# Performance work log

Measured on AMD Instinct MI355X. Metric: run time of the kernel, lower is better.

Reference implementation:

```python
import jax, jax.numpy as jnp
import numpy as np

B, T, C = 16, 512, 32
W = 128            # max_window
SERIES_LEN = 100000
WIN_MIN, WIN_MAX = 2.0, 64.0
SHARP = 1.0        # fixed sharpness of the soft window edge
BN_EPS = 1e-5


def setup_inputs() -> dict:
    key = jax.random.key(0)
    ks = jax.random.split(key, 6)
    x = jax.random.normal(ks[0], (B, T, C), jnp.float32)
    full_series = jax.random.normal(ks[1], (SERIES_LEN, C), jnp.float32)
    # starts >= W so the lookback window never needs padding; end = start + T
    starts = jax.random.randint(ks[2], (B,), W, SERIES_LEN - T)
    indices = jnp.stack([starts, starts + T], axis=1).astype(jnp.int32)  # (B, 2)
    # raw (logit-space) per-channel window sizes, as in the torch init
    raw_win_mean = jax.random.normal(ks[3], (C,), jnp.float32)
    raw_win_std = jax.random.normal(ks[4], (C,), jnp.float32)
    return dict(
        x=x, full_series=full_series, indices=indices,
        raw_win_mean=raw_win_mean, raw_win_std=raw_win_std,
        gamma_mean=jnp.ones((C,), jnp.float32), beta_mean=jnp.zeros((C,), jnp.float32),
        gamma_std=jnp.ones((C,), jnp.float32), beta_std=jnp.zeros((C,), jnp.float32),
    )


def _soft_window_weights(raw_win):
    # sigmoid-mapped window size in [WIN_MIN, WIN_MAX], per channel
    win = WIN_MIN + jax.nn.sigmoid(raw_win) * (WIN_MAX - WIN_MIN)          # (C,)
    age = jnp.arange(W, dtype=jnp.float32)[::-1]                            # slot W-1 is most recent (age 0)
    w = jax.nn.sigmoid(SHARP * (win[None, :] - age[:, None]))               # (W, C)
    return w


def _rolling_windows(full_series, starts):
    # batch_windows[b] = full_series[starts[b]-W : starts[b]+T]   -> (B, W+T, C)
    offs = jnp.arange(W + T)
    bw = full_series[(starts - W)[:, None] + offs[None, :]]                 # (B, W+T, C)
    # window for output step t covers slots [t, t+W) (the W points before the current step)
    tidx = jnp.arange(T)[:, None] + jnp.arange(W)[None, :]                  # (T, W)
    return bw[:, tidx, :]                                                   # (B, T, W, C)


def _batchnorm(f, gamma, beta):
    # BatchNorm1d over (B, C, T): normalize per channel over batch and time, biased var
    mean = f.mean(axis=(0, 1))
    var = ((f - mean) ** 2).mean(axis=(0, 1))
    return (f - mean) * jax.lax.rsqrt(var + BN_EPS) * gamma + beta


def reference(x, full_series, indices, raw_win_mean, raw_win_std,
              gamma_mean, beta_mean, gamma_std, beta_std):
    starts = indices[:, 0]
    xw = _rolling_windows(full_series, starts)                              # (B, T, W, C)

    # feature 1: soft-window weighted mean
    w1 = _soft_window_weights(raw_win_mean)                                 # (W, C)
    s1 = jnp.sum(w1, axis=0)                                                # (C,)
    f_mean = jnp.einsum('btwc,wc->btc', xw, w1) / s1                        # (B, T, C)

    # feature 2: soft-window weighted std
    w2 = _soft_window_weights(raw_win_std)
    s2 = jnp.sum(w2, axis=0)
    m2 = jnp.einsum('btwc,wc->btc', xw, w2) / s2
    var2 = jnp.einsum('btwc,wc->btc', (xw - m2[:, :, None, :]) ** 2, w2) / s2
    f_std = jnp.sqrt(var2 + 1e-8)

    out_mean = _batchnorm(f_mean, gamma_mean, beta_mean)
    out_std = _batchnorm(f_std, gamma_std, beta_std)
    return jnp.concatenate([x, out_mean, out_std], axis=-1)                 # (B, T, 3*C)
```

## Files before the change

### kernel.cpp

```cpp
#include <hip/hip_runtime.h>
#include <math.h>

#define NB 16
#define NT 512
#define NC 32
#define NW 128
#define TILE_T 32
#define NTILES (NT / TILE_T)
#define NBLK (NB * NTILES)
#define NROWS (TILE_T + NW)
#define PADROWS 169
#define NTR 25
#define WIN_MIN_F 2.0f
#define WIN_RANGE_F 62.0f

#define WS_FMEAN 0
#define WS_FSTD  (NB*NT*NC)
#define WS_PART  (2*NB*NT*NC)

typedef float v2f __attribute__((ext_vector_type(2)));

__device__ __forceinline__ float fast_sigmoid_neg(float a) {
    return __builtin_amdgcn_rcpf(1.0f + __expf(a));
}

__global__ __launch_bounds__(256) void feat_main(
    const float* __restrict__ x,
    const float* __restrict__ series,
    const int*   __restrict__ indices,
    const float* __restrict__ rwm,
    const float* __restrict__ rws,
    float* __restrict__ f_mean,
    float* __restrict__ f_std,
    float* __restrict__ partials,
    float* __restrict__ out)
{
    __shared__ __align__(16) float s_x[PADROWS * NC];
    __shared__ __align__(16) v2f   s_P[NROWS * NC];
    __shared__ __align__(16) v2f   s_wt[NTR * NC];
    __shared__ float s_win[2 * NC];
    __shared__ int   s_wsi[2 * NC];
    __shared__ float s_red[1024];

    const int tid = threadIdx.x;
    const int blk = blockIdx.x;
    const int b   = blk >> 4;
    const int tt  = blk & 15;
    const int t0  = tt * TILE_T;
    const int start = indices[2 * b];

    {
        const int row = b * NT + t0 + (tid >> 3);
        const int q = tid & 7;
        ((float4*)out)[row * 24 + q] = ((const float4*)x)[row * 8 + q];
    }

    if (tid < 2 * NC) {
        const int c = tid & 31;
        const float raw = (tid < NC) ? rwm[c] : rws[c];
        const float win = WIN_MIN_F + WIN_RANGE_F * fast_sigmoid_neg(-raw);
        s_win[tid] = win;
        s_wsi[tid] = (int)(115.0f - win);
    }

    const float4* src4 = (const float4*)(series + (size_t)(start - NW + t0) * NC);
    float4* dst4 = (float4*)s_x;
#pragma unroll
    for (int k = 0; k < 5; ++k) {
        const int j = tid + k * 256;
        dst4[j] = src4[j];
    }
    if (tid < 72) {
        dst4[1280 + tid] = make_float4(0.f, 0.f, 0.f, 0.f);
    }
    __syncthreads();

    const int c_s  = tid & 31;
    const int seg  = tid >> 5;
    float l1[20], l2[20];
    {
        float r1 = 0.f, r2 = 0.f;
        const int base = (seg * 20) * NC + c_s;
#pragma unroll
        for (int i = 0; i < 20; ++i) {
            l1[i] = r1; l2[i] = r2;
            const float xv = s_x[base + i * NC];
            r1 += xv;
            r2 = fmaf(xv, xv, r2);
        }
        s_red[0 * 256 + seg * NC + c_s] = r1;
        s_red[1 * 256 + seg * NC + c_s] = r2;
    }

    for (int i = tid; i < 2 * NTR * NC; i += 256) {
        const int c = i & 31;
        const int r = i >> 5;
        const int tbl = (r >= NTR) ? 1 : 0;
        const int j = r - NTR * tbl;
        const int ws = s_wsi[tbl * NC + c];
        const int w = ws + j;
        float val = 0.f;
        if (w < NW) {
            const float age = (float)(NW - 1 - w);
            val = fast_sigmoid_neg(age - s_win[tbl * NC + c]);
        }
        ((float*)s_wt)[(j * NC + c) * 2 + tbl] = val;
    }
    __syncthreads();

    if (tid < 64) {
        const int tbl = tid >> 5, c = tid & 31;
        float o = 0.f;
#pragma unroll
        for (int s = 0; s < 8; ++s) {
            const int idx = tbl * 256 + s * NC + c;
            const float t = s_red[idx];
            s_red[idx] = o;
            o += t;
        }
    }
    __syncthreads();

    {
        const float o1 = s_red[0 * 256 + seg * NC + c_s];
        const float o2 = s_red[1 * 256 + seg * NC + c_s];
#pragma unroll
        for (int i = 0; i < 20; ++i) {
            v2f p; p.x = o1 + l1[i]; p.y = o2 + l2[i];
            s_P[(seg * 20 + i) * NC + c_s] = p;
        }
    }
    __syncthreads();

    const int c  = tid & 31;
    const int rg = tid >> 5;
    const int r0 = rg * 4;
    const int wsm = s_wsi[c];
    const int wss = s_wsi[NC + c];

    float a1[4] = {0.f,0.f,0.f,0.f};
    float a2[4] = {0.f,0.f,0.f,0.f};
    float a3[4] = {0.f,0.f,0.f,0.f};
    float sw1 = 0.f, sw2 = 0.f;

    const int bm_ = (r0 + wsm) * NC + c;
    const int bs_ = (r0 + wss) * NC + c;
    float xm[4], xv[4], qv[4];
#pragma unroll
    for (int k = 0; k < 4; ++k) {
        xm[k] = s_x[bm_ + k * NC];
        const float v = s_x[bs_ + k * NC];
        xv[k] = v; qv[k] = v * v;
    }

#pragma unroll 5
    for (int j = 0; j < NTR; ++j) {
        const v2f wv = s_wt[j * NC + c];
        sw1 += wv.x; sw2 += wv.y;
#pragma unroll
        for (int k = 0; k < 4; ++k) {
            a1[k] = fmaf(xm[k], wv.x, a1[k]);
            a2[k] = fmaf(xv[k], wv.y, a2[k]);
            a3[k] = fmaf(qv[k], wv.y, a3[k]);
        }
        xm[0] = xm[1]; xm[1] = xm[2]; xm[2] = xm[3];
        xm[3] = s_x[bm_ + (4 + j) * NC];
        xv[0] = xv[1]; xv[1] = xv[2]; xv[2] = xv[3];
        qv[0] = qv[1]; qv[1] = qv[2]; qv[2] = qv[3];
        const float nv = s_x[bs_ + (4 + j) * NC];
        xv[3] = nv; qv[3] = nv * nv;
    }

    const int wsm25 = (wsm + NTR < NW) ? wsm + NTR : NW;
    const int wss25 = (wss + NTR < NW) ? wss + NTR : NW;
    const float s1 = sw1 + (float)(NW - wsm25);
    const float s2 = sw2 + (float)(NW - wss25);
    const float inv1 = __builtin_amdgcn_rcpf(s1);
    const float inv2 = __builtin_amdgcn_rcpf(s2);

    float p0 = 0.f, p1 = 0.f, p2 = 0.f, p3 = 0.f;
#pragma unroll
    for (int k = 0; k < 4; ++k) {
        const int t = r0 + k;
        const v2f pe = s_P[(t + NW) * NC + c];
        const v2f pm = s_P[(t + wsm25) * NC + c];
        const v2f ps = s_P[(t + wss25) * NC + c];
        const float A1 = a1[k] + (pe.x - pm.x);
        const float A2 = a2[k] + (pe.x - ps.x);
        const float A3 = a3[k] + (pe.y - ps.y);
        const float fm = A1 * inv1;
        const float m2 = A2 * inv2;
        const float var = fmaxf(A3 * inv2 - m2 * m2, 0.f);
        const float fs = sqrtf(var + 1e-8f);
        const size_t o = ((size_t)(b * NT + t0 + t)) * NC + c;
        f_mean[o] = fm;
        f_std[o]  = fs;
        p0 += fm; p1 = fmaf(fm, fm, p1); p2 += fs; p3 = fmaf(fs, fs, p3);
    }

    s_red[0 * 256 + rg * NC + c] = p0;
    s_red[1 * 256 + rg * NC + c] = p1;
    s_red[2 * 256 + rg * NC + c] = p2;
    s_red[3 * 256 + rg * NC + c] = p3;
    __syncthreads();

    if (tid < 128) {
        const int stat = tid >> 5, cc = tid & 31;
        float s = 0.f;
#pragma unroll
        for (int g = 0; g < 8; ++g) s += s_red[stat * 256 + g * NC + cc];
        partials[blk * (4 * NC) + stat * NC + cc] = s;
    }
}

__global__ __launch_bounds__(256) void bn_write(
    const float* __restrict__ f_mean,
    const float* __restrict__ f_std,
    const float* __restrict__ partials,
    const float* __restrict__ gm, const float* __restrict__ bm,
    const float* __restrict__ gs, const float* __restrict__ bs,
    float* __restrict__ out)
{
    __shared__ __align__(16) float s_part[8 * 128];
    __shared__ __align__(16) float s_sums[128];
    __shared__ __align__(16) float s_coef[4 * NC];

    const int tid = threadIdx.x;

    {
        const int cell  = tid & 31;
        const int slice = tid >> 5;
        const float4* p4 = (const float4*)partials;
        float4 acc = {0.f, 0.f, 0.f, 0.f};
#pragma unroll 8
        for (int i = 0; i < 32; ++i) {
            const float4 v = p4[(slice * 32 + i) * 32 + cell];
            acc.x += v.x; acc.y += v.y; acc.z += v.z; acc.w += v.w;
        }
        *(float4*)&s_part[(slice * 32 + cell) * 4] = acc;
    }
    __syncthreads();
    if (tid < 32) {
        float4 s = {0.f, 0.f, 0.f, 0.f};
#pragma unroll
        for (int sl = 0; sl < 8; ++sl) {
            const float4 v = ((const float4*)s_part)[sl * 32 + tid];
            s.x += v.x; s.y += v.y; s.z += v.z; s.w += v.w;
        }
        ((float4*)s_sums)[tid] = s;
    }
    __syncthreads();
    if (tid < NC) {
        const float invN = 1.0f / (float)(NB * NT);
        const float mu_m  = s_sums[tid] * invN;
        float var_m = s_sums[32 + tid] * invN - mu_m * mu_m;
        var_m = fmaxf(var_m, 0.0f);
        const float A1 = gm[tid] / sqrtf(var_m + 1e-5f);
        const float B1 = bm[tid] - mu_m * A1;
        const float mu_s  = s_sums[64 + tid] * invN;
        float var_s = s_sums[96 + tid] * invN - mu_s * mu_s;
        var_s = fmaxf(var_s, 0.0f);
        const float A2 = gs[tid] / sqrtf(var_s + 1e-5f);
        const float B2 = bs[tid] - mu_s * A2;
        s_coef[tid]          = A1;
        s_coef[NC + tid]     = B1;
        s_coef[2 * NC + tid] = A2;
        s_coef[3 * NC + tid] = B2;
    }
    __syncthreads();

    const float4* fm4 = (const float4*)f_mean;
    const float4* fs4 = (const float4*)f_std;
    const float4* cf4 = (const float4*)s_coef;
    float4* out4 = (float4*)out;
    const int row0 = blockIdx.x * 32;

#pragma unroll
    for (int k = 0; k < 2; ++k) {
        const int j = tid + k * 256;
        const int r = j >> 4;
        const int q = j & 15;
        const int row = row0 + r;
        float4 v;
        int oq;
        if (q < 8) {
            const float4 f = fm4[row * 8 + q];
            const float4 A = cf4[q], Bv = cf4[8 + q];
            v.x = fmaf(f.x, A.x, Bv.x); v.y = fmaf(f.y, A.y, Bv.y);
            v.z = fmaf(f.z, A.z, Bv.z); v.w = fmaf(f.w, A.w, Bv.w);
            oq = 8 + q;
        } else {
            const int m = q - 8;
            const float4 f = fs4[row * 8 + m];
            const float4 A = cf4[16 + m], Bv = cf4[24 + m];
            v.x = fmaf(f.x, A.x, Bv.x); v.y = fmaf(f.y, A.y, Bv.y);
            v.z = fmaf(f.z, A.z, Bv.z); v.w = fmaf(f.w, A.w, Bv.w);
            oq = 16 + m;
        }
        out4[row * 24 + oq] = v;
    }
}

extern "C" void kernel_launch(void* const* d_in, const int* in_sizes, int n_in,
                              void* d_out, int out_size, void* d_ws, size_t ws_size,
                              hipStream_t stream) {
    const float* x      = (const float*)d_in[0];
    const float* series = (const float*)d_in[1];
    const int*   idx    = (const int*)d_in[2];
    const float* rwm    = (const float*)d_in[3];
    const float* rws    = (const float*)d_in[4];
    const float* gm     = (const float*)d_in[5];
    const float* bm     = (const float*)d_in[6];
    const float* gs     = (const float*)d_in[7];
    const float* bs     = (const float*)d_in[8];
    float* out = (float*)d_out;
    float* ws  = (float*)d_ws;

    float* f_mean   = ws + WS_FMEAN;
    float* f_std    = ws + WS_FSTD;
    float* partials = ws + WS_PART;

    feat_main<<<NBLK, 256, 0, stream>>>(x, series, idx, rwm, rws, f_mean, f_std, partials, out);
    bn_write<<<NBLK, 256, 0, stream>>>(f_mean, f_std, partials, gm, bm, gs, bs, out);
}
```

Measured before the change: 15.08 us.

## Fuse feature and batchnorm kernels via grid-wide atomic barrier

New measurement: 30.61 us. 2.03x slower.

```diff
diff --git a/kernel.cpp b/kernel.cpp
--- a/kernel.cpp
+++ b/kernel.cpp
@@ -14,25 +14,22 @@
 #define WIN_MIN_F 2.0f
 #define WIN_RANGE_F 62.0f
 
-#define WS_FMEAN 0
-#define WS_FSTD  (NB*NT*NC)
-#define WS_PART  (2*NB*NT*NC)
-
 typedef float v2f __attribute__((ext_vector_type(2)));
 
 __device__ __forceinline__ float fast_sigmoid_neg(float a) {
     return __builtin_amdgcn_rcpf(1.0f + __expf(a));
 }
 
-__global__ __launch_bounds__(256) void feat_main(
+__global__ __launch_bounds__(256) void feat_fused(
     const float* __restrict__ x,
     const float* __restrict__ series,
     const int*   __restrict__ indices,
     const float* __restrict__ rwm,
     const float* __restrict__ rws,
-    float* __restrict__ f_mean,
-    float* __restrict__ f_std,
+    const float* __restrict__ gm, const float* __restrict__ bm,
+    const float* __restrict__ gs, const float* __restrict__ bs,
     float* __restrict__ partials,
+    unsigned int* __restrict__ ctr,
     float* __restrict__ out)
 {
     __shared__ __align__(16) float s_x[PADROWS * NC];
@@ -40,7 +37,9 @@
     __shared__ __align__(16) v2f   s_wt[NTR * NC];
     __shared__ float s_win[2 * NC];
     __shared__ int   s_wsi[2 * NC];
-    __shared__ float s_red[1024];
+    __shared__ __align__(16) float s_red[1024];
+    __shared__ __align__(16) float s_sums[128];
+    __shared__ __align__(16) float s_coef[128];
 
     const int tid = threadIdx.x;
     const int blk = blockIdx.x;
@@ -178,6 +177,7 @@
     const float inv1 = __builtin_amdgcn_rcpf(s1);
     const float inv2 = __builtin_amdgcn_rcpf(s2);
 
+    float fm[4], fs[4];
     float p0 = 0.f, p1 = 0.f, p2 = 0.f, p3 = 0.f;
 #pragma unroll
     for (int k = 0; k < 4; ++k) {
@@ -188,14 +188,11 @@
         const float A1 = a1[k] + (pe.x - pm.x);
         const float A2 = a2[k] + (pe.x - ps.x);
         const float A3 = a3[k] + (pe.y - ps.y);
-        const float fm = A1 * inv1;
+        fm[k] = A1 * inv1;
         const float m2 = A2 * inv2;
         const float var = fmaxf(A3 * inv2 - m2 * m2, 0.f);
-        const float fs = sqrtf(var + 1e-8f);
-        const size_t o = ((size_t)(b * NT + t0 + t)) * NC + c;
-        f_mean[o] = fm;
-        f_std[o]  = fs;
-        p0 += fm; p1 = fmaf(fm, fm, p1); p2 += fs; p3 = fmaf(fs, fs, p3);
+        fs[k] = sqrtf(var + 1e-8f);
+        p0 += fm[k]; p1 = fmaf(fm[k], fm[k], p1); p2 += fs[k]; p3 = fmaf(fs[k], fs[k], p3);
     }
 
     s_red[0 * 256 + rg * NC + c] = p0;
@@ -211,21 +208,17 @@
         for (int g = 0; g < 8; ++g) s += s_red[stat * 256 + g * NC + cc];
         partials[blk * (4 * NC) + stat * NC + cc] = s;
     }
-}
-
-__global__ __launch_bounds__(256) void bn_write(
-    const float* __restrict__ f_mean,
-    const float* __restrict__ f_std,
-    const float* __restrict__ partials,
-    const float* __restrict__ gm, const float* __restrict__ bm,
-    const float* __restrict__ gs, const float* __restrict__ bs,
-    float* __restrict__ out)
-{
-    __shared__ __align__(16) float s_part[8 * 128];
-    __shared__ __align__(16) float s_sums[128];
-    __shared__ __align__(16) float s_coef[4 * NC];
-
-    const int tid = threadIdx.x;
+    __syncthreads();
+
+    if (tid == 0) {
+        __hip_atomic_fetch_add(ctr, 1u, __ATOMIC_ACQ_REL, __HIP_MEMORY_SCOPE_AGENT);
+        unsigned int guard = 0;
+        while (__hip_atomic_load(ctr, __ATOMIC_ACQUIRE, __HIP_MEMORY_SCOPE_AGENT) < (unsigned)NBLK) {
+            __builtin_amdgcn_s_sleep(8);
+            if (++guard > 100000000u) break;
+        }
+    }
+    __syncthreads();
 
     {
         const int cell  = tid & 31;
@@ -237,14 +230,14 @@
             const float4 v = p4[(slice * 32 + i) * 32 + cell];
             acc.x += v.x; acc.y += v.y; acc.z += v.z; acc.w += v.w;
         }
-        *(float4*)&s_part[(slice * 32 + cell) * 4] = acc;
+        *(float4*)&s_red[(slice * 32 + cell) * 4] = acc;
     }
     __syncthreads();
     if (tid < 32) {
         float4 s = {0.f, 0.f, 0.f, 0.f};
 #pragma unroll
         for (int sl = 0; sl < 8; ++sl) {
-            const float4 v = ((const float4*)s_part)[sl * 32 + tid];
+            const float4 v = ((const float4*)s_red)[sl * 32 + tid];
             s.x += v.x; s.y += v.y; s.z += v.z; s.w += v.w;
         }
         ((float4*)s_sums)[tid] = s;
@@ -253,51 +246,27 @@
     if (tid < NC) {
         const float invN = 1.0f / (float)(NB * NT);
         const float mu_m  = s_sums[tid] * invN;
-        float var_m = s_sums[32 + tid] * invN - mu_m * mu_m;
-        var_m = fmaxf(var_m, 0.0f);
+        float var_m = fmaxf(s_sums[32 + tid] * invN - mu_m * mu_m, 0.0f);
         const float A1 = gm[tid] / sqrtf(var_m + 1e-5f);
         const float B1 = bm[tid] - mu_m * A1;
         const float mu_s  = s_sums[64 + tid] * invN;
-        float var_s = s_sums[96 + tid] * invN - mu_s * mu_s;
-        var_s = fmaxf(var_s, 0.0f);
+        float var_s = fmaxf(s_sums[96 + tid] * invN - mu_s * mu_s, 0.0f);
         const float A2 = gs[tid] / sqrtf(var_s + 1e-5f);
         const float B2 = bs[tid] - mu_s * A2;
-        s_coef[tid]          = A1;
-        s_coef[NC + tid]     = B1;
-        s_coef[2 * NC + tid] = A2;
-        s_coef[3 * NC + tid] = B2;
-    }
-    __syncthreads();
-
-    const float4* fm4 = (const float4*)f_mean;
-    const float4* fs4 = (const float4*)f_std;
-    const float4* cf4 = (const float4*)s_coef;
-    float4* out4 = (float4*)out;
-    const int row0 = blockIdx.x * 32;
-
-#pragma unroll
-    for (int k = 0; k < 2; ++k) {
-        const int j = tid + k * 256;
-        const int r = j >> 4;
-        const int q = j & 15;
-        const int row = row0 + r;
-        float4 v;
-        int oq;
-        if (q < 8) {
-            const float4 f = fm4[row * 8 + q];
-            const float4 A = cf4[q], Bv = cf4[8 + q];
-            v.x = fmaf(f.x, A.x, Bv.x); v.y = fmaf(f.y, A.y, Bv.y);
-            v.z = fmaf(f.z, A.z, Bv.z); v.w = fmaf(f.w, A.w, Bv.w);
-            oq = 8 + q;
-        } else {
-            const int m = q - 8;
-            const float4 f = fs4[row * 8 + m];
-            const float4 A = cf4[16 + m], Bv = cf4[24 + m];
-            v.x = fmaf(f.x, A.x, Bv.x); v.y = fmaf(f.y, A.y, Bv.y);
-            v.z = fmaf(f.z, A.z, Bv.z); v.w = fmaf(f.w, A.w, Bv.w);
-            oq = 16 + m;
-        }
-        out4[row * 24 + oq] = v;
+        s_coef[tid]      = A1;
+        s_coef[32 + tid] = B1;
+        s_coef[64 + tid] = A2;
+        s_coef[96 + tid] = B2;
+    }
+    __syncthreads();
+
+    const float A1 = s_coef[c],      B1 = s_coef[32 + c];
+    const float A2 = s_coef[64 + c], B2 = s_coef[96 + c];
+#pragma unroll
+    for (int k = 0; k < 4; ++k) {
+        const size_t o = ((size_t)(b * NT + t0 + r0 + k)) * 96;
+        out[o + 32 + c] = fmaf(fm[k], A1, B1);
+        out[o + 64 + c] = fmaf(fs[k], A2, B2);
     }
 }
 
@@ -316,10 +285,10 @@
     float* out = (float*)d_out;
     float* ws  = (float*)d_ws;
 
-    float* f_mean   = ws + WS_FMEAN;
-    float* f_std    = ws + WS_FSTD;
-    float* partials = ws + WS_PART;
-
-    feat_main<<<NBLK, 256, 0, stream>>>(x, series, idx, rwm, rws, f_mean, f_std, partials, out);
-    bn_write<<<NBLK, 256, 0, stream>>>(f_mean, f_std, partials, gm, bm, gs, bs, out);
+    float* partials   = ws;
+    unsigned int* ctr = (unsigned int*)(ws + NBLK * 4 * NC);
+
+    hipMemsetAsync(ctr, 0, sizeof(unsigned int), stream);
+    feat_fused<<<NBLK, 256, 0, stream>>>(x, series, idx, rwm, rws,
+                                         gm, bm, gs, bs, partials, ctr, out);
 }
```
